# Optimization experiments

Measured on AMD Instinct MI355X. Metric: run time of the kernel, lower is better.

The kernel has to match this reference:

```python
import jax, jax.numpy as jnp
import numpy as np

HEAD_NUM = 8
ATT_DIM = 64
NUM_UNITS = HEAD_NUM * ATT_DIM  # 512
B, T, D = 8, 1024, NUM_UNITS
NEG_BIG = -2.0**32 + 1.0


def _sinusoidal_table(max_len, num_hidden):
    P = np.zeros((1, max_len, num_hidden), dtype=np.float32)
    X = np.arange(max_len, dtype=np.float32).reshape(-1, 1) / np.power(
        10000.0, np.arange(0, num_hidden, 2, dtype=np.float32) / num_hidden)
    P[:, :, 0::2] = np.sin(X)
    P[:, :, 1::2] = np.cos(X)
    return P


def setup_inputs() -> dict:
    key = jax.random.key(0)
    ks = jax.random.split(key, 8)
    w_scale = 0.02
    return {
        "queries": jax.random.normal(ks[0], (B, T, D), dtype=jnp.float32),
        "keys": jax.random.normal(ks[1], (B, T, D), dtype=jnp.float32),
        "query_masks": jnp.ones((B, T), dtype=jnp.float32),
        "key_masks": jnp.ones((B, T), dtype=jnp.float32),
        "pos_table": jnp.asarray(_sinusoidal_table(T, D)),
        "W_Query": jax.random.normal(ks[2], (D, D), dtype=jnp.float32) * w_scale,
        "W_key": jax.random.normal(ks[3], (D, D), dtype=jnp.float32) * w_scale,
        "W_Value": jax.random.normal(ks[4], (D, D), dtype=jnp.float32) * w_scale,
        "fw1": jax.random.normal(ks[5], (D, 4 * D), dtype=jnp.float32) * w_scale,
        "fw2": jax.random.normal(ks[6], (4 * D, D), dtype=jnp.float32) * w_scale,
    }


def reference(queries, keys, query_masks, key_masks, pos_table,
              W_Query, W_key, W_Value, fw1, fw2):
    h, dh = HEAD_NUM, ATT_DIM
    pe_scale = jnp.asarray(NUM_UNITS ** 0.5, dtype=queries.dtype)
    pos = pos_table[:, :queries.shape[1], :] * pe_scale  # scale=True
    q_in = queries + pos
    k_in = keys + pos

    q = jnp.einsum('btd,de->bte', q_in, W_Query)
    k = jnp.einsum('btd,de->bte', k_in, W_key)
    # Faithful to source: values computed from the projected keys.
    v = jnp.einsum('btd,de->bte', k, W_Value)

    # split heads: (B,T,h*dh) -> (h,B,T,dh)
    def heads(x):
        return x.reshape(B, T, h, dh).transpose(2, 0, 1, 3)
    qh, kh, vh = heads(q), heads(k), heads(v)

    scores = jnp.einsum('hbqd,hbkd->hbqk', qh, kh) / (dh ** 0.5)
    # key padding mask
    scores = jnp.where(key_masks[None, :, None, :] == 1.0, scores, NEG_BIG)
    # blinding: mask the diagonal
    eye = jnp.eye(T, dtype=bool)
    scores = jnp.where(eye[None, None, :, :], NEG_BIG, scores)
    attn = jax.nn.softmax(scores, axis=-1)
    attn = attn * query_masks[None, :, :, None]

    out = jnp.einsum('hbqk,hbkd->hbqd', attn, vh)
    result = out.transpose(1, 2, 0, 3).reshape(B, T, D)  # merge heads

    result = result + q_in  # residual (use_res, queries after PE)

    # feed-forward with residual
    hidden = jax.nn.relu(jnp.einsum('btd,df->btf', result, fw1))
    ffn = jnp.einsum('btf,fd->btd', hidden, fw2)
    result = result + ffn

    # output_type == 'mean'
    return jnp.mean(result, axis=1, keepdims=True)  # (B,1,D)
```

## Files before the change

### kernel.cpp

```cpp
#include <hip/hip_runtime.h>


typedef __bf16 bf16x8 __attribute__((ext_vector_type(8)));
typedef __bf16 bf16x4 __attribute__((ext_vector_type(4)));
typedef float f32x4 __attribute__((ext_vector_type(4)));
typedef unsigned short u16x8 __attribute__((ext_vector_type(8)));
typedef unsigned short u16x4 __attribute__((ext_vector_type(4)));

#define MFMA_BF16(a, b, c) __builtin_amdgcn_mfma_f32_16x16x32_bf16((a), (b), (c), 0, 0, 0)
#define NEGBIG (-4294967295.0f)
#define QSCALE 0.18033688011112042f
#define EXP2(x) __builtin_amdgcn_exp2f(x)

#define GLL16(g, l)                                                                 \
    __builtin_amdgcn_global_load_lds((__attribute__((address_space(1))) void*)(g),  \
                                     (__attribute__((address_space(3))) void*)(l),  \
                                     16, 0, 0)

static __device__ __forceinline__ unsigned short f2bf(float f) {
    __bf16 h = (__bf16)f;
    return __builtin_bit_cast(unsigned short, h);
}
static __device__ __forceinline__ float bf2f(unsigned short h) {
    return __builtin_bit_cast(float, ((unsigned int)h) << 16);
}

__global__ __launch_bounds__(256) void prep_kernel(
    const float* __restrict__ q, const float* __restrict__ k,
    const float* __restrict__ pos,
    unsigned short* __restrict__ qo, unsigned short* __restrict__ ko)
{
    size_t i = ((size_t)blockIdx.x * 256 + threadIdx.x) * 4;
    size_t td = i & (size_t)(1024 * 512 - 1);
    float4 qv = *(const float4*)(q + i);
    float4 kv = *(const float4*)(k + i);
    float4 pv = *(const float4*)(pos + td);
    const float S = 22.627416997969522f;
    u16x4 qr, kr;
    qr[0] = f2bf(qv.x + pv.x * S); qr[1] = f2bf(qv.y + pv.y * S);
    qr[2] = f2bf(qv.z + pv.z * S); qr[3] = f2bf(qv.w + pv.w * S);
    kr[0] = f2bf(kv.x + pv.x * S); kr[1] = f2bf(kv.y + pv.y * S);
    kr[2] = f2bf(kv.z + pv.z * S); kr[3] = f2bf(kv.w + pv.w * S);
    *(u16x4*)(qo + i) = qr;
    *(u16x4*)(ko + i) = kr;
}

__global__ __launch_bounds__(256) void wconv_kernel(
    const float* __restrict__ w0, const float* __restrict__ w1, const float* __restrict__ w2,
    const float* __restrict__ w3, const float* __restrict__ w4,
    unsigned short* __restrict__ o0, unsigned short* __restrict__ o1, unsigned short* __restrict__ o2,
    unsigned short* __restrict__ o3, unsigned short* __restrict__ o4,
    unsigned short* __restrict__ wkp)
{
    int id = blockIdx.x;
    const float* in; unsigned short* out; int K, N, kt, nt; bool dup = false;
    if (id < 768) {
        int m = id >> 8; id &= 255;
        in  = (m == 0) ? w0 : ((m == 1) ? w1 : w2);
        out = (m == 0) ? o0 : ((m == 1) ? o1 : o2);
        dup = (m == 1);
        K = 512; N = 512; kt = id >> 4; nt = id & 15;
    } else if (id < 1792) {
        id -= 768; in = w3; out = o3; K = 512; N = 2048; kt = id >> 6; nt = id & 63;
    } else {
        id -= 1792; in = w4; out = o4; K = 2048; N = 512; kt = id >> 4; nt = id & 15;
    }
    int k0 = kt * 32, n0 = nt * 32;
    __shared__ float tile[32][33];
    int tx = threadIdx.x & 31, ty = threadIdx.x >> 5;
#pragma unroll
    for (int i = 0; i < 32; i += 8) {
        float v = in[(size_t)(k0 + ty + i) * N + n0 + tx];
        tile[ty + i][tx] = v;
        if (dup) wkp[(size_t)(k0 + ty + i) * 512 + n0 + tx] = f2bf(v);
    }
    __syncthreads();
#pragma unroll
    for (int i = 0; i < 32; i += 8)
        out[(size_t)(n0 + ty + i) * K + k0 + tx] = f2bf(tile[tx][ty + i]);
}

__global__ __launch_bounds__(256) void gemm64(
    const unsigned short* __restrict__ A, const unsigned short* __restrict__ Bt,
    unsigned short* __restrict__ C, int N, int K)
{
    __shared__ unsigned short As[64 * 32];
    __shared__ unsigned short Bs[64 * 32];
    const int tid = threadIdx.x;
    const int wave = tid >> 6, lane = tid & 63;
    const int g = lane >> 4, lr = lane & 15;
    const int wm = (wave >> 1) * 32, wn = (wave & 1) * 32;
    const size_t bm = (size_t)blockIdx.x * 64, bn = (size_t)blockIdx.y * 64;
    const int row = tid >> 2, kc = (tid & 3) * 8;
    const unsigned short* Ap = A + (bm + row) * (size_t)K + kc;
    const unsigned short* Bp = Bt + (bn + row) * (size_t)K + kc;
    unsigned short* AsW = As + tid * 8;
    unsigned short* BsW = Bs + tid * 8;

    f32x4 acc[2][2] = {};
    for (int k0 = 0; k0 < K; k0 += 32) {
        __syncthreads();
        GLL16(Ap + k0, AsW);
        GLL16(Bp + k0, BsW);
        __syncthreads();
        bf16x8 af[2], bfr[2];
#pragma unroll
        for (int t = 0; t < 2; ++t) {
            af[t]  = *(const bf16x8*)&As[(wm + t * 16 + lr) * 32 + g * 8];
            bfr[t] = *(const bf16x8*)&Bs[(wn + t * 16 + lr) * 32 + g * 8];
        }
#pragma unroll
        for (int i = 0; i < 2; ++i)
#pragma unroll
            for (int j = 0; j < 2; ++j)
                acc[i][j] = MFMA_BF16(af[i], bfr[j], acc[i][j]);
    }
#pragma unroll
    for (int i = 0; i < 2; ++i)
#pragma unroll
        for (int j = 0; j < 2; ++j) {
            size_t rr = bm + wm + i * 16 + g * 4;
            size_t cc = bn + wn + j * 16 + lr;
#pragma unroll
            for (int r = 0; r < 4; ++r)
                C[(rr + r) * (size_t)N + cc] = f2bf(acc[i][j][r]);
        }
}

static __device__ __forceinline__ void gemm_core(
    const unsigned short* __restrict__ A,
    const unsigned short* __restrict__ Bt,
    unsigned short* __restrict__ C,
    int N, int K, int mode,
    unsigned short* As, unsigned short* Bs, int bx, int by)
{
    const int tid = threadIdx.x;
    const int wave = tid >> 6, lane = tid & 63;
    const int g = lane >> 4, lr = lane & 15;
    const int wm = (wave >> 1) * 64, wn = (wave & 1) * 64;
    const size_t bm = (size_t)bx * 128, bn = (size_t)by * 128;

    const int srow = tid >> 2, skc = (tid & 3) * 8;
    const unsigned short* Ap = A + (bm + srow) * (size_t)K + skc;
    const unsigned short* Bp = Bt + (bn + srow) * (size_t)K + skc;

    f32x4 acc[4][4] = {};
    for (int k0 = 0; k0 < K; k0 += 64) {
        __syncthreads();
        GLL16(Ap + k0,                        As + tid * 8);
        GLL16(Ap + (size_t)64 * K + k0,       As + 2048 + tid * 8);
        GLL16(Ap + k0 + 32,                   As + 4096 + tid * 8);
        GLL16(Ap + (size_t)64 * K + k0 + 32,  As + 6144 + tid * 8);
        GLL16(Bp + k0,                        Bs + tid * 8);
        GLL16(Bp + (size_t)64 * K + k0,       Bs + 2048 + tid * 8);
        GLL16(Bp + k0 + 32,                   Bs + 4096 + tid * 8);
        GLL16(Bp + (size_t)64 * K + k0 + 32,  Bs + 6144 + tid * 8);
        __syncthreads();
#pragma unroll
        for (int kk = 0; kk < 2; ++kk) {
            bf16x8 af[4], bfr[4];
#pragma unroll
            for (int t = 0; t < 4; ++t) {
                af[t]  = *(const bf16x8*)&As[kk * 4096 + (wm + t * 16 + lr) * 32 + g * 8];
                bfr[t] = *(const bf16x8*)&Bs[kk * 4096 + (wn + t * 16 + lr) * 32 + g * 8];
            }
#pragma unroll
            for (int rt = 0; rt < 4; ++rt)
#pragma unroll
                for (int ct = 0; ct < 4; ++ct)
                    acc[rt][ct] = MFMA_BF16(af[rt], bfr[ct], acc[rt][ct]);
        }
    }

#pragma unroll
    for (int rt = 0; rt < 4; ++rt)
#pragma unroll
        for (int ct = 0; ct < 4; ++ct) {
            size_t row = bm + wm + rt * 16 + g * 4;
            size_t col = bn + wn + ct * 16 + lr;
#pragma unroll
            for (int r = 0; r < 4; ++r) {
                float x = acc[rt][ct][r];
                if (mode == 2) x *= QSCALE;
                C[(row + r) * (size_t)N + col] = f2bf(x);
            }
        }
}

__global__ __launch_bounds__(256, 2) void proj3_kernel(
    const unsigned short* __restrict__ q_in, const unsigned short* __restrict__ k_in,
    const unsigned short* __restrict__ wqt, const unsigned short* __restrict__ wkt,
    const unsigned short* __restrict__ wkvt,
    unsigned short* __restrict__ qb, unsigned short* __restrict__ kb,
    unsigned short* __restrict__ vb)
{
    __shared__ unsigned short As[128 * 64];
    __shared__ unsigned short Bs[128 * 64];
    const unsigned short *A, *Bt; unsigned short* C; int mode = 0;
    switch (blockIdx.z) {
        case 0:  A = q_in; Bt = wqt;  C = qb; mode = 2; break;
        case 1:  A = k_in; Bt = wkt;  C = kb; break;
        default: A = k_in; Bt = wkvt; C = vb; break;
    }
    gemm_core(A, Bt, C, 512, 512, mode, As, Bs, blockIdx.x, blockIdx.y);
}

__global__ __launch_bounds__(256, 2) void ffn1_mean(
    const unsigned short* __restrict__ A,
    const unsigned short* __restrict__ Bt,
    float* __restrict__ hmean)
{
    __shared__ unsigned short As[128 * 64];
    __shared__ unsigned short Bs[128 * 64];
    const int tid = threadIdx.x;
    const int wave = tid >> 6, lane = tid & 63;
    const int g = lane >> 4, lr = lane & 15;
    const int wm = (wave >> 1) * 64, wn = (wave & 1) * 64;
    const size_t bm = (size_t)blockIdx.x * 128, bn = (size_t)blockIdx.y * 128;

    const int srow = tid >> 2, skc = (tid & 3) * 8;
    const unsigned short* Ap = A + (bm + srow) * (size_t)512 + skc;
    const unsigned short* Bp = Bt + (bn + srow) * (size_t)512 + skc;

    f32x4 acc[4][4] = {};
    for (int k0 = 0; k0 < 512; k0 += 64) {
        __syncthreads();
        GLL16(Ap + k0,                         As + tid * 8);
        GLL16(Ap + (size_t)64 * 512 + k0,      As + 2048 + tid * 8);
        GLL16(Ap + k0 + 32,                    As + 4096 + tid * 8);
        GLL16(Ap + (size_t)64 * 512 + k0 + 32, As + 6144 + tid * 8);
        GLL16(Bp + k0,                         Bs + tid * 8);
        GLL16(Bp + (size_t)64 * 512 + k0,      Bs + 2048 + tid * 8);
        GLL16(Bp + k0 + 32,                    Bs + 4096 + tid * 8);
        GLL16(Bp + (size_t)64 * 512 + k0 + 32, Bs + 6144 + tid * 8);
        __syncthreads();
#pragma unroll
        for (int kk = 0; kk < 2; ++kk) {
            bf16x8 af[4], bfr[4];
#pragma unroll
            for (int t = 0; t < 4; ++t) {
                af[t]  = *(const bf16x8*)&As[kk * 4096 + (wm + t * 16 + lr) * 32 + g * 8];
                bfr[t] = *(const bf16x8*)&Bs[kk * 4096 + (wn + t * 16 + lr) * 32 + g * 8];
            }
#pragma unroll
            for (int rt = 0; rt < 4; ++rt)
#pragma unroll
                for (int ct = 0; ct < 4; ++ct)
                    acc[rt][ct] = MFMA_BF16(af[rt], bfr[ct], acc[rt][ct]);
        }
    }

    const int b = blockIdx.x >> 3;
#pragma unroll
    for (int ct = 0; ct < 4; ++ct) {
        float s = 0.f;
#pragma unroll
        for (int rt = 0; rt < 4; ++rt)
#pragma unroll
            for (int r = 0; r < 4; ++r) s += fmaxf(acc[rt][ct][r], 0.f);
        s += __shfl_xor(s, 16, 64);
        s += __shfl_xor(s, 32, 64);
        if (g == 0)
            atomicAdd(hmean + b * 2048 + bn + wn + ct * 16 + lr, s);
    }
}

__global__ __launch_bounds__(256) void ffn2_small(
    const float* __restrict__ hmean, const unsigned short* __restrict__ fw2t,
    float* __restrict__ out)
{
    __shared__ float red[256];
    const int b = blockIdx.x;
    const int d = blockIdx.y * 64 + (threadIdx.x & 63);
    const int fs = (threadIdx.x >> 6) * 512;
    const float* hm = hmean + b * 2048 + fs;
    const unsigned short* wr = fw2t + (size_t)d * 2048 + fs;
    float acc = 0.f;
    for (int f = 0; f < 512; f += 8) {
        u16x8 w = *(const u16x8*)(wr + f);
        f32x4 h0 = *(const f32x4*)(hm + f);
        f32x4 h1 = *(const f32x4*)(hm + f + 4);
        acc += h0[0] * bf2f(w[0]) + h0[1] * bf2f(w[1]) + h0[2] * bf2f(w[2]) + h0[3] * bf2f(w[3])
             + h1[0] * bf2f(w[4]) + h1[1] * bf2f(w[5]) + h1[2] * bf2f(w[6]) + h1[3] * bf2f(w[7]);
    }
    red[threadIdx.x] = acc;
    __syncthreads();
    if (threadIdx.x < 64) {
        float s = red[threadIdx.x] + red[threadIdx.x + 64] +
                  red[threadIdx.x + 128] + red[threadIdx.x + 192];
        out[b * 512 + d] += s * (1.0f / 1024.0f);
    }
}

__global__ __launch_bounds__(512, 2) void attn_kernel(
    const unsigned short* __restrict__ Q,
    const unsigned short* __restrict__ Kp,
    const unsigned short* __restrict__ V,
    const float* __restrict__ queries,
    const float* __restrict__ pos,
    const float* __restrict__ kmask,
    const float* __restrict__ qmask,
    unsigned short* __restrict__ Res,
    float* __restrict__ out)
{
    __shared__ unsigned short Ks[2][64 * 72];
    __shared__ unsigned short Vts[2][64 * 72];
    __shared__ unsigned short Ps[8][16 * 72];
    __shared__ float kbias[1024];
    const int tid = threadIdx.x, wave = tid >> 6, lane = tid & 63;
    const int g = lane >> 4, lr = lane & 15;
    const int b = blockIdx.x >> 3, h = blockIdx.x & 7;
    const int qg = blockIdx.y * 128 + wave * 16 + lr;

    for (int i = tid; i < 1024; i += 512)
        kbias[i] = (kmask[b * 1024 + i] == 1.0f) ? 0.f : NEGBIG;

    bf16x8 aq0, aq1;
    {
        const unsigned short* qp = Q + ((size_t)(b * 1024 + qg)) * 512 + h * 64 + g * 8;
        aq0 = *(const bf16x8*)qp;
        aq1 = *(const bf16x8*)(qp + 32);
    }
    const float qm = qmask[b * 1024 + qg];

    float m_run = -3.0e38f, l_run = 0.f;
    f32x4 o[4] = {};

    const unsigned short* kbase = Kp + ((size_t)(b * 1024)) * 512 + h * 64;
    const unsigned short* vbase = V + ((size_t)(b * 1024)) * 512 + h * 64;

    const int half = tid >> 8;
    const int skey = (tid & 255) >> 2, sd = (tid & 3) * 16;
    const int vk0 = (tid & 15) * 4, vd0 = ((tid >> 4) & 15) * 4;

    u16x8 kr0, kr1; u16x4 vr[4];
    if (half) {
        const unsigned short* kp = kbase + (size_t)skey * 512 + sd;
        kr0 = *(const u16x8*)kp; kr1 = *(const u16x8*)(kp + 8);
    } else {
        const unsigned short* vp = vbase + (size_t)vk0 * 512 + vd0;
#pragma unroll
        for (int j = 0; j < 4; ++j) vr[j] = *(const u16x4*)(vp + (size_t)j * 512);
    }
    if (half) {
        *(u16x8*)&Ks[0][skey * 72 + sd] = kr0;
        *(u16x8*)&Ks[0][skey * 72 + sd + 8] = kr1;
    } else {
#pragma unroll
        for (int i = 0; i < 4; ++i) {
            u16x4 w = { vr[0][i], vr[1][i], vr[2][i], vr[3][i] };
            *(u16x4*)&Vts[0][(vd0 + i) * 72 + vk0] = w;
        }
    }
    if (half) {
        const unsigned short* kp = kbase + (size_t)(64 + skey) * 512 + sd;
        kr0 = *(const u16x8*)kp; kr1 = *(const u16x8*)(kp + 8);
    } else {
        const unsigned short* vp = vbase + (size_t)(64 + vk0) * 512 + vd0;
#pragma unroll
        for (int j = 0; j < 4; ++j) vr[j] = *(const u16x4*)(vp + (size_t)j * 512);
    }
    __syncthreads();

    for (int it = 0; it < 16; ++it) {
        const int j0 = it * 64;
        const unsigned short* Kc = Ks[it & 1];
        const unsigned short* Vc = Vts[it & 1];

        f32x4 s[4];
#pragma unroll
        for (int ct = 0; ct < 4; ++ct) {
            bf16x8 ka = *(const bf16x8*)&Kc[(ct * 16 + lr) * 72 + g * 8];
            bf16x8 kc = *(const bf16x8*)&Kc[(ct * 16 + lr) * 72 + 32 + g * 8];
            f32x4 z = {};
            z = MFMA_BF16(ka, aq0, z);
            s[ct] = MFMA_BF16(kc, aq1, z);
        }

#pragma unroll
        for (int ct = 0; ct < 4; ++ct)
            s[ct] += *(const f32x4*)&kbias[j0 + ct * 16 + g * 4];
        if (((qg ^ j0) & ~63) == 0) {
#pragma unroll
            for (int ct = 0; ct < 4; ++ct) {
                unsigned diff = (unsigned)(qg - (j0 + ct * 16 + g * 4));
                if (diff < 4u) s[ct][diff] = NEGBIG;
            }
        }
        float rmax = -3.0e38f;
#pragma unroll
        for (int ct = 0; ct < 4; ++ct)
#pragma unroll
            for (int r = 0; r < 4; ++r) rmax = fmaxf(rmax, s[ct][r]);
        rmax = fmaxf(rmax, __shfl_xor(rmax, 16, 64));
        rmax = fmaxf(rmax, __shfl_xor(rmax, 32, 64));

        float mn = fmaxf(m_run, rmax);
        float alpha = EXP2(m_run - mn);
        m_run = mn;
        float psum = 0.f;
#pragma unroll
        for (int ct = 0; ct < 4; ++ct) {
            f32x4 p;
#pragma unroll
            for (int r = 0; r < 4; ++r) { p[r] = EXP2(s[ct][r] - mn); psum += p[r]; }
            bf16x4 pk = { (__bf16)p[0], (__bf16)p[1], (__bf16)p[2], (__bf16)p[3] };
            *(bf16x4*)&Ps[wave][lr * 72 + ct * 16 + g * 4] = pk;
        }
        psum += __shfl_xor(psum, 16, 64);
        psum += __shfl_xor(psum, 32, 64);
        l_run = l_run * alpha + psum;
#pragma unroll
        for (int dt = 0; dt < 4; ++dt) o[dt] *= alpha;

        bf16x8 p0 = *(const bf16x8*)&Ps[wave][lr * 72 + g * 8];
        bf16x8 p1 = *(const bf16x8*)&Ps[wave][lr * 72 + 32 + g * 8];
#pragma unroll
        for (int dt = 0; dt < 4; ++dt) {
            bf16x8 va = *(const bf16x8*)&Vc[(dt * 16 + lr) * 72 + g * 8];
            bf16x8 vc = *(const bf16x8*)&Vc[(dt * 16 + lr) * 72 + 32 + g * 8];
            o[dt] = MFMA_BF16(va, p0, o[dt]);
            o[dt] = MFMA_BF16(vc, p1, o[dt]);
        }

        if (it + 1 < 16) {
            unsigned short* Kn = Ks[(it + 1) & 1];
            unsigned short* Vn = Vts[(it + 1) & 1];
            if (half) {
                *(u16x8*)&Kn[skey * 72 + sd] = kr0;
                *(u16x8*)&Kn[skey * 72 + sd + 8] = kr1;
            } else {
#pragma unroll
                for (int i = 0; i < 4; ++i) {
                    u16x4 w = { vr[0][i], vr[1][i], vr[2][i], vr[3][i] };
                    *(u16x4*)&Vn[(vd0 + i) * 72 + vk0] = w;
                }
            }
        }
        if (it + 2 < 16) {
            const int jn = (it + 2) * 64;
            if (half) {
                const unsigned short* kp = kbase + (size_t)(jn + skey) * 512 + sd;
                kr0 = *(const u16x8*)kp; kr1 = *(const u16x8*)(kp + 8);
            } else {
                const unsigned short* vp = vbase + (size_t)(jn + vk0) * 512 + vd0;
#pragma unroll
                for (int j = 0; j < 4; ++j) vr[j] = *(const u16x4*)(vp + (size_t)j * 512);
            }
        }
        __syncthreads();
    }

    const float inv_l = 1.0f / l_run;
    const float S = 22.627416997969522f;
    float vals[4][4];
#pragma unroll
    for (int dt = 0; dt < 4; ++dt) {
        size_t col = (size_t)h * 64 + dt * 16 + g * 4;
        size_t idx = ((size_t)(b * 1024 + qg)) * 512 + col;
        f32x4 qv = *(const f32x4*)&queries[idx];
        f32x4 pv = *(const f32x4*)&pos[(size_t)qg * 512 + col];
        u16x4 wr;
#pragma unroll
        for (int r = 0; r < 4; ++r) {
            float v = o[dt][r] * inv_l * qm + qv[r] + pv[r] * S;
            vals[dt][r] = v;
            wr[r] = f2bf(v);
        }
        *(u16x4*)&Res[idx] = wr;
    }

    float* red = kbias;
#pragma unroll
    for (int dt = 0; dt < 4; ++dt)
#pragma unroll
        for (int r = 0; r < 4; ++r) {
            float x = vals[dt][r];
            x += __shfl_xor(x, 1, 64);
            x += __shfl_xor(x, 2, 64);
            x += __shfl_xor(x, 4, 64);
            x += __shfl_xor(x, 8, 64);
            if (lr == 0) red[wave * 64 + dt * 16 + g * 4 + r] = x;
        }
    __syncthreads();
    if (tid < 64) {
        float s = 0.f;
#pragma unroll
        for (int w = 0; w < 8; ++w) s += red[w * 64 + tid];
        atomicAdd(out + b * 512 + h * 64 + tid, s * (1.0f / 1024.0f));
    }
}

extern "C" void kernel_launch(void* const* d_in, const int* in_sizes, int n_in,
                              void* d_out, int out_size, void* d_ws, size_t ws_size,
                              hipStream_t stream)
{
    (void)in_sizes; (void)n_in; (void)out_size; (void)ws_size;
    const float* queries     = (const float*)d_in[0];
    const float* keys        = (const float*)d_in[1];
    const float* query_masks = (const float*)d_in[2];
    const float* key_masks   = (const float*)d_in[3];
    const float* pos_table   = (const float*)d_in[4];
    const float* W_Query     = (const float*)d_in[5];
    const float* W_key       = (const float*)d_in[6];
    const float* W_Value     = (const float*)d_in[7];
    const float* fw1         = (const float*)d_in[8];
    const float* fw2         = (const float*)d_in[9];
    float* out = (float*)d_out;

    unsigned short* ws = (unsigned short*)d_ws;
    const size_t NE = (size_t)8 * 1024 * 512;
    unsigned short* q_in   = ws;
    unsigned short* k_in   = ws + NE;
    unsigned short* qb     = ws + 2 * NE;
    unsigned short* kb     = ws + 3 * NE;
    unsigned short* vb     = ws + 4 * NE;
    unsigned short* result = q_in;
    unsigned short* wqt    = ws + 6 * NE;
    unsigned short* wkt    = wqt + 512 * 512;
    unsigned short* wvt    = wkt + 512 * 512;
    unsigned short* fw1t   = wvt + 512 * 512;
    unsigned short* fw2t   = fw1t + 2048 * 512;
    unsigned short* wkp    = fw2t + 2048 * 512;
    unsigned short* wkvt   = wkp + 512 * 512;
    float*          hmean  = (float*)(wkvt + 512 * 512);

    hipMemsetAsync(d_out, 0, 8 * 512 * sizeof(float), stream);
    hipMemsetAsync(hmean, 0, 8 * 2048 * sizeof(float), stream);
    prep_kernel<<<4096, 256, 0, stream>>>(queries, keys, pos_table, q_in, k_in);
    wconv_kernel<<<2816, 256, 0, stream>>>(W_Query, W_key, W_Value, fw1, fw2,
                                           wqt, wkt, wvt, fw1t, fw2t, wkp);
    gemm64<<<dim3(8, 8), 256, 0, stream>>>(wvt, wkp, wkvt, 512, 512);
    proj3_kernel<<<dim3(64, 4, 3), 256, 0, stream>>>(q_in, k_in, wqt, wkt, wkvt, qb, kb, vb);
    attn_kernel<<<dim3(64, 8), 512, 0, stream>>>(qb, kb, vb, queries, pos_table,
                                                 key_masks, query_masks, result, out);
    ffn1_mean<<<dim3(64, 16), 256, 0, stream>>>(result, fw1t, hmean);
    ffn2_small<<<dim3(8, 8), 256, 0, stream>>>(hmean, fw2t, out);
}
```

Baseline: 213.9 us.

## Process two query tiles per wave in attention and fold memsets into prep

Each attention wave now handles 32 queries (two 16-row tiles) instead of 16, so every K/V tile loaded into shared memory is reused twice as much and the grid is halved. The launch-bounds occupancy hint is dropped to allow the larger register footprint. The two hipMemsetAsync calls are removed, and the first blocks of prep_kernel zero the output and hmean buffers instead, saving two launches. Risks are higher register pressure, fewer blocks (256) to fill the GPU, and less latency hiding.

```diff
diff --git a/kernel.cpp b/kernel.cpp
--- a/kernel.cpp
+++ b/kernel.cpp
@@ -28,8 +28,16 @@
 __global__ __launch_bounds__(256) void prep_kernel(
     const float* __restrict__ q, const float* __restrict__ k,
     const float* __restrict__ pos,
-    unsigned short* __restrict__ qo, unsigned short* __restrict__ ko)
-{
+    unsigned short* __restrict__ qo, unsigned short* __restrict__ ko,
+    float* __restrict__ out, float* __restrict__ hmean)
+{
+    if (blockIdx.x < 5) {
+        float* dst = (blockIdx.x == 0) ? out : hmean + (blockIdx.x - 1) * 4096;
+        float4 z = {0.f, 0.f, 0.f, 0.f};
+#pragma unroll
+        for (int j = 0; j < 4; ++j)
+            *(float4*)(dst + threadIdx.x * 16 + j * 4) = z;
+    }
     size_t i = ((size_t)blockIdx.x * 256 + threadIdx.x) * 4;
     size_t td = i & (size_t)(1024 * 512 - 1);
     float4 qv = *(const float4*)(q + i);
@@ -292,7 +300,7 @@
     }
 }
 
-__global__ __launch_bounds__(512, 2) void attn_kernel(
+__global__ __launch_bounds__(512) void attn_kernel(
     const unsigned short* __restrict__ Q,
     const unsigned short* __restrict__ Kp,
     const unsigned short* __restrict__ V,
@@ -305,26 +313,29 @@
 {
     __shared__ unsigned short Ks[2][64 * 72];
     __shared__ unsigned short Vts[2][64 * 72];
-    __shared__ unsigned short Ps[8][16 * 72];
+    __shared__ unsigned short Ps[8][2][16 * 72];
     __shared__ float kbias[1024];
     const int tid = threadIdx.x, wave = tid >> 6, lane = tid & 63;
     const int g = lane >> 4, lr = lane & 15;
     const int b = blockIdx.x >> 3, h = blockIdx.x & 7;
-    const int qg = blockIdx.y * 128 + wave * 16 + lr;
+    const int qg0 = blockIdx.y * 256 + wave * 32 + lr;
 
     for (int i = tid; i < 1024; i += 512)
         kbias[i] = (kmask[b * 1024 + i] == 1.0f) ? 0.f : NEGBIG;
 
-    bf16x8 aq0, aq1;
-    {
-        const unsigned short* qp = Q + ((size_t)(b * 1024 + qg)) * 512 + h * 64 + g * 8;
-        aq0 = *(const bf16x8*)qp;
-        aq1 = *(const bf16x8*)(qp + 32);
-    }
-    const float qm = qmask[b * 1024 + qg];
-
-    float m_run = -3.0e38f, l_run = 0.f;
-    f32x4 o[4] = {};
+    bf16x8 aq[2][2];
+    float qm[2], m_run[2], l_run[2];
+    f32x4 o[2][4];
+#pragma unroll
+    for (int u = 0; u < 2; ++u) {
+        const unsigned short* qp = Q + ((size_t)(b * 1024 + qg0 + u * 16)) * 512 + h * 64 + g * 8;
+        aq[u][0] = *(const bf16x8*)qp;
+        aq[u][1] = *(const bf16x8*)(qp + 32);
+        qm[u] = qmask[b * 1024 + qg0 + u * 16];
+        m_run[u] = -3.0e38f; l_run[u] = 0.f;
+#pragma unroll
+        for (int dt = 0; dt < 4; ++dt) o[u][dt] = (f32x4){0.f, 0.f, 0.f, 0.f};
+    }
 
     const unsigned short* kbase = Kp + ((size_t)(b * 1024)) * 512 + h * 64;
     const unsigned short* vbase = V + ((size_t)(b * 1024)) * 512 + h * 64;
@@ -367,60 +378,66 @@
         const unsigned short* Kc = Ks[it & 1];
         const unsigned short* Vc = Vts[it & 1];
 
-        f32x4 s[4];
-#pragma unroll
-        for (int ct = 0; ct < 4; ++ct) {
-            bf16x8 ka = *(const bf16x8*)&Kc[(ct * 16 + lr) * 72 + g * 8];
-            bf16x8 kc = *(const bf16x8*)&Kc[(ct * 16 + lr) * 72 + 32 + g * 8];
-            f32x4 z = {};
-            z = MFMA_BF16(ka, aq0, z);
-            s[ct] = MFMA_BF16(kc, aq1, z);
-        }
-
-#pragma unroll
-        for (int ct = 0; ct < 4; ++ct)
-            s[ct] += *(const f32x4*)&kbias[j0 + ct * 16 + g * 4];
-        if (((qg ^ j0) & ~63) == 0) {
+        f32x4 s[2][4];
+#pragma unroll
+        for (int u = 0; u < 2; ++u)
 #pragma unroll
             for (int ct = 0; ct < 4; ++ct) {
-                unsigned diff = (unsigned)(qg - (j0 + ct * 16 + g * 4));
-                if (diff < 4u) s[ct][diff] = NEGBIG;
-            }
-        }
-        float rmax = -3.0e38f;
-#pragma unroll
-        for (int ct = 0; ct < 4; ++ct)
-#pragma unroll
-            for (int r = 0; r < 4; ++r) rmax = fmaxf(rmax, s[ct][r]);
-        rmax = fmaxf(rmax, __shfl_xor(rmax, 16, 64));
-        rmax = fmaxf(rmax, __shfl_xor(rmax, 32, 64));
-
-        float mn = fmaxf(m_run, rmax);
-        float alpha = EXP2(m_run - mn);
-        m_run = mn;
-        float psum = 0.f;
-#pragma unroll
-        for (int ct = 0; ct < 4; ++ct) {
-            f32x4 p;
-#pragma unroll
-            for (int r = 0; r < 4; ++r) { p[r] = EXP2(s[ct][r] - mn); psum += p[r]; }
-            bf16x4 pk = { (__bf16)p[0], (__bf16)p[1], (__bf16)p[2], (__bf16)p[3] };
-            *(bf16x4*)&Ps[wave][lr * 72 + ct * 16 + g * 4] = pk;
-        }
-        psum += __shfl_xor(psum, 16, 64);
-        psum += __shfl_xor(psum, 32, 64);
-        l_run = l_run * alpha + psum;
-#pragma unroll
-        for (int dt = 0; dt < 4; ++dt) o[dt] *= alpha;
-
-        bf16x8 p0 = *(const bf16x8*)&Ps[wave][lr * 72 + g * 8];
-        bf16x8 p1 = *(const bf16x8*)&Ps[wave][lr * 72 + 32 + g * 8];
-#pragma unroll
-        for (int dt = 0; dt < 4; ++dt) {
-            bf16x8 va = *(const bf16x8*)&Vc[(dt * 16 + lr) * 72 + g * 8];
-            bf16x8 vc = *(const bf16x8*)&Vc[(dt * 16 + lr) * 72 + 32 + g * 8];
-            o[dt] = MFMA_BF16(va, p0, o[dt]);
-            o[dt] = MFMA_BF16(vc, p1, o[dt]);
+                bf16x8 ka = *(const bf16x8*)&Kc[(ct * 16 + lr) * 72 + g * 8];
+                bf16x8 kc = *(const bf16x8*)&Kc[(ct * 16 + lr) * 72 + 32 + g * 8];
+                f32x4 z = {};
+                z = MFMA_BF16(ka, aq[u][0], z);
+                s[u][ct] = MFMA_BF16(kc, aq[u][1], z);
+            }
+
+#pragma unroll
+        for (int u = 0; u < 2; ++u) {
+            const int qgu = qg0 + u * 16;
+#pragma unroll
+            for (int ct = 0; ct < 4; ++ct)
+                s[u][ct] += *(const f32x4*)&kbias[j0 + ct * 16 + g * 4];
+            if (((qgu ^ j0) & ~63) == 0) {
+#pragma unroll
+                for (int ct = 0; ct < 4; ++ct) {
+                    unsigned diff = (unsigned)(qgu - (j0 + ct * 16 + g * 4));
+                    if (diff < 4u) s[u][ct][diff] = NEGBIG;
+                }
+            }
+            float rmax = -3.0e38f;
+#pragma unroll
+            for (int ct = 0; ct < 4; ++ct)
+#pragma unroll
+                for (int r = 0; r < 4; ++r) rmax = fmaxf(rmax, s[u][ct][r]);
+            rmax = fmaxf(rmax, __shfl_xor(rmax, 16, 64));
+            rmax = fmaxf(rmax, __shfl_xor(rmax, 32, 64));
+
+            float mn = fmaxf(m_run[u], rmax);
+            float alpha = EXP2(m_run[u] - mn);
+            m_run[u] = mn;
+            float psum = 0.f;
+#pragma unroll
+            for (int ct = 0; ct < 4; ++ct) {
+                f32x4 p;
+#pragma unroll
+                for (int r = 0; r < 4; ++r) { p[r] = EXP2(s[u][ct][r] - mn); psum += p[r]; }
+                bf16x4 pk = { (__bf16)p[0], (__bf16)p[1], (__bf16)p[2], (__bf16)p[3] };
+                *(bf16x4*)&Ps[wave][u][lr * 72 + ct * 16 + g * 4] = pk;
+            }
+            psum += __shfl_xor(psum, 16, 64);
+            psum += __shfl_xor(psum, 32, 64);
+            l_run[u] = l_run[u] * alpha + psum;
+#pragma unroll
+            for (int dt = 0; dt < 4; ++dt) o[u][dt] *= alpha;
+
+            bf16x8 p0 = *(const bf16x8*)&Ps[wave][u][lr * 72 + g * 8];
+            bf16x8 p1 = *(const bf16x8*)&Ps[wave][u][lr * 72 + 32 + g * 8];
+#pragma unroll
+            for (int dt = 0; dt < 4; ++dt) {
+                bf16x8 va = *(const bf16x8*)&Vc[(dt * 16 + lr) * 72 + g * 8];
+                bf16x8 vc = *(const bf16x8*)&Vc[(dt * 16 + lr) * 72 + 32 + g * 8];
+                o[u][dt] = MFMA_BF16(va, p0, o[u][dt]);
+                o[u][dt] = MFMA_BF16(vc, p1, o[u][dt]);
+            }
         }
 
         if (it + 1 < 16) {
@@ -451,31 +468,35 @@
         __syncthreads();
     }
 
-    const float inv_l = 1.0f / l_run;
     const float S = 22.627416997969522f;
-    float vals[4][4];
-#pragma unroll
-    for (int dt = 0; dt < 4; ++dt) {
-        size_t col = (size_t)h * 64 + dt * 16 + g * 4;
-        size_t idx = ((size_t)(b * 1024 + qg)) * 512 + col;
-        f32x4 qv = *(const f32x4*)&queries[idx];
-        f32x4 pv = *(const f32x4*)&pos[(size_t)qg * 512 + col];
-        u16x4 wr;
+    float vals[2][4][4];
+#pragma unroll
+    for (int u = 0; u < 2; ++u) {
+        const float inv_l = 1.0f / l_run[u];
+        const int qgu = qg0 + u * 16;
+#pragma unroll
+        for (int dt = 0; dt < 4; ++dt) {
+            size_t col = (size_t)h * 64 + dt * 16 + g * 4;
+            size_t idx = ((size_t)(b * 1024 + qgu)) * 512 + col;
+            f32x4 qv = *(const f32x4*)&queries[idx];
+            f32x4 pv = *(const f32x4*)&pos[(size_t)qgu * 512 + col];
+            u16x4 wr;
+#pragma unroll
+            for (int r = 0; r < 4; ++r) {
+                float v = o[u][dt][r] * inv_l * qm[u] + qv[r] + pv[r] * S;
+                vals[u][dt][r] = v;
+                wr[r] = f2bf(v);
+            }
+            *(u16x4*)&Res[idx] = wr;
+        }
+    }
+
+    float* red = kbias;
+#pragma unroll
+    for (int dt = 0; dt < 4; ++dt)
 #pragma unroll
         for (int r = 0; r < 4; ++r) {
-            float v = o[dt][r] * inv_l * qm + qv[r] + pv[r] * S;
-            vals[dt][r] = v;
-            wr[r] = f2bf(v);
-        }
-        *(u16x4*)&Res[idx] = wr;
-    }
-
-    float* red = kbias;
-#pragma unroll
-    for (int dt = 0; dt < 4; ++dt)
-#pragma unroll
-        for (int r = 0; r < 4; ++r) {
-            float x = vals[dt][r];
+            float x = vals[0][dt][r] + vals[1][dt][r];
             x += __shfl_xor(x, 1, 64);
             x += __shfl_xor(x, 2, 64);
             x += __shfl_xor(x, 4, 64);
@@ -525,14 +546,12 @@
     unsigned short* wkvt   = wkp + 512 * 512;
     float*          hmean  = (float*)(wkvt + 512 * 512);
 
-    hipMemsetAsync(d_out, 0, 8 * 512 * sizeof(float), stream);
-    hipMemsetAsync(hmean, 0, 8 * 2048 * sizeof(float), stream);
-    prep_kernel<<<4096, 256, 0, stream>>>(queries, keys, pos_table, q_in, k_in);
+    prep_kernel<<<4096, 256, 0, stream>>>(queries, keys, pos_table, q_in, k_in, out, hmean);
     wconv_kernel<<<2816, 256, 0, stream>>>(W_Query, W_key, W_Value, fw1, fw2,
                                            wqt, wkt, wvt, fw1t, fw2t, wkp);
     gemm64<<<dim3(8, 8), 256, 0, stream>>>(wvt, wkp, wkvt, 512, 512);
     proj3_kernel<<<dim3(64, 4, 3), 256, 0, stream>>>(q_in, k_in, wqt, wkt, wkvt, qb, kb, vb);
-    attn_kernel<<<dim3(64, 8), 512, 0, stream>>>(qb, kb, vb, queries, pos_table,
+    attn_kernel<<<dim3(64, 4), 512, 0, stream>>>(qb, kb, vb, queries, pos_table,
                                                  key_masks, query_masks, result, out);
     ffn1_mean<<<dim3(64, 16), 256, 0, stream>>>(result, fw1t, hmean);
     ffn2_small<<<dim3(8, 8), 256, 0, stream>>>(hmean, fw2t, out);
```

After: 207.1 us. 1.03x faster.
